# Optimization experiments

Measured on AMD Instinct MI355X. Metric: run time of the kernel, lower is better.

The kernel has to match this reference:

```python
import jax, jax.numpy as jnp
import numpy as np

N, M, P = 16, 4, 8
BSZ, T = 256, 256
STD_DYN, STD_OBS = 0.1, 0.1


def setup_inputs() -> dict:
    key = jax.random.key(0)
    ks = jax.random.split(key, 5)
    Y = jax.random.normal(ks[0], (BSZ, T, P), dtype=jnp.float32)
    U = jax.random.normal(ks[1], (BSZ, T, M), dtype=jnp.float32)
    # stable time-varying dynamics (spectral radius < 1)
    A_seq = 0.85 * jnp.eye(N, dtype=jnp.float32) + 0.02 * jax.random.normal(ks[2], (T, N, N), dtype=jnp.float32)
    B_seq = 0.1 * jax.random.normal(ks[3], (T, N, M), dtype=jnp.float32)
    C_seq = jax.random.normal(ks[4], (T, P, N), dtype=jnp.float32) / np.float32(np.sqrt(N))
    mu0 = jnp.zeros((N,), dtype=jnp.float32)
    Sigma0 = jnp.eye(N, dtype=jnp.float32)
    return dict(Y=Y, U=U, A_seq=A_seq, B_seq=B_seq, C_seq=C_seq, mu0=mu0, Sigma0=Sigma0)


def _sym(x):
    return 0.5 * (x + jnp.swapaxes(x, -1, -2))


def reference(Y, U, A_seq, B_seq, C_seq, mu0, Sigma0):
    B, T_, p = Y.shape
    n = mu0.shape[0]
    Q = (STD_DYN ** 2) * jnp.eye(n, dtype=Y.dtype)
    R = (STD_OBS ** 2) * jnp.eye(p, dtype=Y.dtype)
    I = jnp.eye(n, dtype=Y.dtype)
    Yt = jnp.swapaxes(Y, 0, 1)  # [T,B,p] time-major for scan
    Ut = jnp.swapaxes(U, 0, 1)  # [T,B,m]

    def filt_step(carry, xs):
        mu, Sig = carry                      # [B,n], [B,n,n]
        y_t, u_t, A, Bm, C = xs
        mu_pred = mu @ A.T + u_t @ Bm.T      # [B,n]
        Sig_pred = jnp.einsum('ij,bjk,lk->bil', A, Sig, A) + Q
        r = y_t - mu_pred @ C.T              # innovation [B,p]
        S = _sym(jnp.einsum('ij,bjk,lk->bil', C, Sig_pred, C) + R)
        PCT = Sig_pred @ C.T                 # [B,n,p]
        K = jnp.swapaxes(jnp.linalg.solve(S, jnp.swapaxes(PCT, -1, -2)), -1, -2)  # [B,n,p]
        mu_f = mu_pred + jnp.einsum('bnp,bp->bn', K, r)
        I_KC = I - K @ C                     # [B,n,n]
        Sig_f = _sym(jnp.einsum('bij,bjk,blk->bil', I_KC, Sig_pred, I_KC)
                     + jnp.einsum('bip,pq,bjq->bij', K, R, K))
        return (mu_f, Sig_f), (mu_f, Sig_f, mu_pred, Sig_pred)

    mu_init = jnp.broadcast_to(mu0, (B, n))
    Sig_init = jnp.broadcast_to(Sigma0, (B, n, n))
    _, (mus_f, Sigs_f, mus_p, Sigs_p) = jax.lax.scan(
        filt_step, (mu_init, Sig_init), (Yt, Ut, A_seq, B_seq, C_seq))

    def smooth_step(carry, xs):
        mu_next, Sig_next = carry            # smoothed t+1
        mu_f, Sig_f, mu_p_next, Sig_p_next, A_next = xs
        SfAT = jnp.einsum('bij,kj->bik', Sig_f, A_next)  # Sigma_t|t A_{t+1}^T
        J = jnp.swapaxes(jnp.linalg.solve(jnp.swapaxes(Sig_p_next, -1, -2),
                                          jnp.swapaxes(SfAT, -1, -2)), -1, -2)
        mu_s = mu_f + jnp.einsum('bij,bj->bi', J, mu_next - mu_p_next)
        Sig_s = _sym(Sig_f + jnp.einsum('bij,bjk,blk->bil', J, Sig_next - Sig_p_next, J))
        return (mu_s, Sig_s), (mu_s, Sig_s)

    carry0 = (mus_f[-1], Sigs_f[-1])
    xs = (mus_f[:-1], Sigs_f[:-1], mus_p[1:], Sigs_p[1:], A_seq[1:])
    _, (mus_s, Sigs_s) = jax.lax.scan(smooth_step, carry0, xs, reverse=True)
    mus_smooth = jnp.concatenate([mus_s, mus_f[-1:]], axis=0)    # [T,B,n]
    Sigs_smooth = jnp.concatenate([Sigs_s, Sigs_f[-1:]], axis=0)  # [T,B,n,n]

    return (jnp.swapaxes(mus_smooth, 0, 1),   # [B,T,n]
            jnp.swapaxes(Sigs_smooth, 0, 1),  # [B,T,n,n]
            jnp.swapaxes(mus_f, 0, 1),        # [B,T,n]
            jnp.swapaxes(Sigs_f, 0, 1))       # [B,T,n,n]
```

## Files before the change

kernel.cpp:

```cpp
#include <hip/hip_runtime.h>

#define NS 16
#define MD 4
#define PD 8
#define BB 256
#define TL 256
#define QV 0.01f
#define RV 0.01f
#define NCHF 256
#define WF   14
#define NCHS 256
#define WSS  14
#define CHM  8
#define NCHM 32
#define WMU  26

#define WSYNC() do { asm volatile("s_waitcnt lgkmcnt(0)" ::: "memory"); \
                     __builtin_amdgcn_sched_barrier(0); } while (0)

#define Z4 make_float4(0.f, 0.f, 0.f, 0.f)

__device__ __forceinline__ float f4c(const float4 v, int i) {
    return i == 0 ? v.x : i == 1 ? v.y : i == 2 ? v.z : v.w;
}

__global__ __launch_bounds__(256, 1) void kPre(
    const float* __restrict__ A_seq, const float* __restrict__ C_seq,
    float* __restrict__ E_ws, float* __restrict__ SQ_ws)
{
    const int t = blockIdx.x, tid = threadIdx.x;
    __shared__ float sA[16][17], sC[8][17];
    sA[tid >> 4][tid & 15] = A_seq[t * 256 + tid];
    if (tid < 128) sC[tid >> 4][tid & 15] = C_seq[t * 128 + tid];
    __syncthreads();
    if (tid < 128) {
        const int p = tid >> 4, j = tid & 15;
        float a = 0.f;
        #pragma unroll
        for (int k = 0; k < 16; ++k) a += sC[p][k] * sA[k][j];
        E_ws[t * 128 + tid] = a;
    } else if (tid < 192) {
        const int q2 = tid - 128, p = q2 >> 3, q = q2 & 7;
        float a = 0.f;
        #pragma unroll
        for (int k = 0; k < 16; ++k) a += sC[p][k] * sC[q][k];
        SQ_ws[t * 64 + q2] = QV * a + ((p == q) ? RV : 0.f);
    }
}

__global__ __launch_bounds__(64, 1) void kF3_warm(
    const float* __restrict__ A_seq, const float* __restrict__ C_seq,
    const float* __restrict__ E_ws, const float* __restrict__ SQ_ws,
    const float* __restrict__ Sig0,
    float* __restrict__ K_ws, float* __restrict__ Sigf_ws,
    float* __restrict__ Sigp_ws)
{
    const int tlo = blockIdx.x;
    int t0 = tlo - WF; if (t0 < 0) t0 = 0;
    const int nst = tlo + 1 - t0;

    const int l  = threadIdx.x;
    const int r  = l >> 2;
    const int q  = l & 3;
    const int c0 = q * 4;
    const int rc  = l >> 3;
    const int cc0 = (l & 7) * 2;
    const int c8  = l & 7;

    __shared__ float lA[2][16][20];
    __shared__ float lCc[2][8][20];
    __shared__ float lEe[2][8][20];
    __shared__ float lSQs[2][64];
    __shared__ float lSg[2][16][20];
    __shared__ float lT[16][20];
    __shared__ float lW[8][20];
    __shared__ float lCS[8][20];
    __shared__ float lS[64];
    __shared__ float lV[16][20];

    float4 sig4;
    if (t0 == 0) {
        sig4 = *(const float4*)(Sig0 + l * 4);
    } else {
        sig4 = make_float4(r == c0 ? 1.f : 0.f, r == c0 + 1 ? 1.f : 0.f,
                           r == c0 + 2 ? 1.f : 0.f, r == c0 + 3 ? 1.f : 0.f);
    }
    float4 a_c  = *(const float4*)(A_seq + t0 * 256 + l * 4);
    float2 cc_c = *(const float2*)(C_seq + t0 * 128 + l * 2);
    float2 e_c  = *(const float2*)(E_ws  + t0 * 128 + l * 2);
    float  sq_c = SQ_ws[t0 * 64 + l];

    for (int s = 0; s < nst; ++s) {
        const int t = t0 + s;
        const int pb = s & 1;
        const bool commit = (t == tlo);

        *(float4*)&lA[pb][r][c0]   = a_c;
        *(float2*)&lCc[pb][rc][cc0] = cc_c;
        *(float2*)&lEe[pb][rc][cc0] = e_c;
        lSQs[pb][l] = sq_c;
        *(float4*)&lSg[pb][r][c0]  = sig4;
        WSYNC();
        if (s + 1 < nst) {
            a_c  = *(const float4*)(A_seq + (t + 1) * 256 + l * 4);
            cc_c = *(const float2*)(C_seq + (t + 1) * 128 + l * 2);
            e_c  = *(const float2*)(E_ws  + (t + 1) * 128 + l * 2);
            sq_c = SQ_ws[(t + 1) * 64 + l];
        }

        float t4[4] = {0.f, 0.f, 0.f, 0.f};
        #pragma unroll
        for (int kk = 0; kk < 4; ++kk) {
            const float4 a4 = *(const float4*)&lA[pb][r][4 * kk];
            #pragma unroll
            for (int i2 = 0; i2 < 4; ++i2) {
                const float av = f4c(a4, i2);
                const float4 sv = *(const float4*)&lSg[pb][4 * kk + i2][c0];
                t4[0] += av * sv.x; t4[1] += av * sv.y;
                t4[2] += av * sv.z; t4[3] += av * sv.w;
            }
        }
        float w2x = 0.f, w2y = 0.f;
        {
            float4 er[4];
            #pragma unroll
            for (int kk = 0; kk < 4; ++kk) er[kk] = *(const float4*)&lEe[pb][rc][4 * kk];
            #pragma unroll
            for (int kk = 0; kk < 4; ++kk)
                #pragma unroll
                for (int i2 = 0; i2 < 4; ++i2) {
                    const float ev = f4c(er[kk], i2);
                    const float2 s2 = *(const float2*)&lSg[pb][4 * kk + i2][cc0];
                    w2x += ev * s2.x; w2y += ev * s2.y;
                }
        }
        *(float4*)&lT[r][c0]   = make_float4(t4[0], t4[1], t4[2], t4[3]);
        *(float2*)&lW[rc][cc0] = make_float2(w2x, w2y);
        WSYNC();

        float4 trr[4], wrow[4];
// ... 63 lines not shown
                    Lm[r2][c2] = s2 * Dinv[c2];
                }
            }
            float yv[8];
            #pragma unroll
            for (int c2 = 0; c2 < 8; ++c2) {
                float sAcc = lCS[c2][r];
                #pragma unroll
                for (int k2 = 0; k2 < 8; ++k2) if (k2 < c2) sAcc -= Lm[c2][k2] * yv[k2];
                yv[c2] = sAcc * Dinv[c2];
            }
            #pragma unroll
            for (int c2 = 7; c2 >= 0; --c2) {
                float sAcc = yv[c2];
                #pragma unroll
                for (int k2 = 0; k2 < 8; ++k2) if (k2 > c2) sAcc -= Lm[k2][c2] * x[k2];
                x[c2] = sAcc * Dinv[c2];
            }
        }
        float u[4] = { sp[0], sp[1], sp[2], sp[3] };
        #pragma unroll
        for (int p = 0; p < 8; ++p) {
            const float kv = x[p];
            const float4 cs4 = *(const float4*)&lCS[p][c0];
            u[0] -= kv * cs4.x; u[1] -= kv * cs4.y;
            u[2] -= kv * cs4.z; u[3] -= kv * cs4.w;
        }

        if (!commit) {
            sig4 = make_float4(u[0], u[1], u[2], u[3]);
        } else {
            if (q == 0)      *(float4*)(K_ws + t * 128 + r * 8)     = make_float4(x[0], x[1], x[2], x[3]);
            else if (q == 1) *(float4*)(K_ws + t * 128 + r * 8 + 4) = make_float4(x[4], x[5], x[6], x[7]);
            *(float4*)&lV[r][c0] = make_float4(u[0], u[1], u[2], u[3]);
            WSYNC();
            float o[4];
            #pragma unroll
            for (int i = 0; i < 4; ++i) o[i] = 0.5f * (u[i] + lV[c0 + i][r]);
            sig4 = make_float4(o[0], o[1], o[2], o[3]);
            *(float4*)(Sigf_ws + t * 256 + l * 4) = sig4;
        }
    }
}

__global__ __launch_bounds__(256, 1) void kBG(
    const float* __restrict__ A_seq, const float* __restrict__ B_seq,
    const float* __restrict__ C_seq, const float* __restrict__ K_ws,
    const float* __restrict__ Sigf_ws, const float* __restrict__ Sigp_ws,
    float* __restrict__ J_ws, float* __restrict__ G_ws,
    float* __restrict__ Bt2_ws)
{
    const int t = blockIdx.x, tid = threadIdx.x;
    const int i = tid >> 4, j = tid & 15;
    const bool doJ = (t < TL - 1);

    __shared__ float sA0[16][17], sCm[8][17], sKm[16][9], sBm[16][5];
    __shared__ float sCA[8][17], sCB[8][5];
    __shared__ float sSf[16][17], sA1[16][17], sFA[16][17];
    __shared__ float P[2][16][33];

    sA0[i][j] = A_seq[t * 256 + tid];
    if (tid < 128) {
        sCm[tid >> 4][tid & 15] = C_seq[t * 128 + tid];
        sKm[tid >> 3][tid & 7]  = K_ws[t * 128 + tid];
    }
    if (tid < 64) sBm[tid >> 2][tid & 3] = B_seq[t * 64 + tid];
    if (doJ) {
        sSf[i][j] = Sigf_ws[t * 256 + tid];
        sA1[i][j] = A_seq[(t + 1) * 256 + tid];
        P[0][i][j]      = Sigp_ws[(t + 1) * 256 + tid];
        P[0][i][j + 16] = (i == j) ? 1.f : 0.f;
    }
    __syncthreads();

    if (tid < 128) {
        const int p = tid >> 4, jj = tid & 15;
        float a = 0.f;
        #pragma unroll
        for (int k = 0; k < 16; ++k) a += sCm[p][k] * sA0[k][jj];
        sCA[p][jj] = a;
    } else if (tid < 160) {
        const int qq = tid - 128, p = qq >> 2, m = qq & 3;
        float a = 0.f;
        #pragma unroll
        for (int k = 0; k < 16; ++k) a += sCm[p][k] * sBm[k][m];
        sCB[p][m] = a;
    }
    if (doJ) {
        float fa = 0.f;
        #pragma unroll
        for (int k = 0; k < 16; ++k) fa += sSf[i][k] * sA1[j][k];
        sFA[i][j] = fa;
    }
    __syncthreads();

    float gv = sA0[i][j];
    #pragma unroll
    for (int p = 0; p < 8; ++p) gv -= sKm[i][p] * sCA[p][j];
    G_ws[t * 256 + tid] = gv;
    if (tid < 64) {
        const int ii = tid >> 2, m = tid & 3;
        float bv = sBm[ii][m];
        #pragma unroll
        for (int p = 0; p < 8; ++p) bv -= sKm[ii][p] * sCB[p][m];
        Bt2_ws[t * 64 + tid] = bv;
    }

    if (doJ) {
        #pragma unroll 1
        for (int k = 0; k < 16; ++k) {
            const int cur = k & 1, nxt = cur ^ 1;
            const float akk = P[cur][k][k];
            const float piv = 1.f / akk;
            const float rkj  = P[cur][k][j];
            const float rkj2 = P[cur][k][j + 16];
            if (i == k) {
                P[nxt][i][j]      = rkj * piv;
                P[nxt][i][j + 16] = rkj2 * piv;
            } else {
                const float f = P[cur][i][k] * piv;
                P[nxt][i][j]      = P[cur][i][j]      - f * rkj;
                P[nxt][i][j + 16] = P[cur][i][j + 16] - f * rkj2;
            }
            __syncthreads();
        }
        float acc = 0.f;
        #pragma unroll
        for (int k = 0; k < 16; ++k) acc += sFA[i][k] * P[0][k][16 + j];
        J_ws[t * 256 + tid] = acc;
    }
}

__global__ __launch_bounds__(256, 1) void kES3(
    const float* __restrict__ A_seq, const float* __restrict__ B_seq,
    const float* __restrict__ U, const float* __restrict__ Y,
    const float* __restrict__ mu0,
    const float* __restrict__ G_ws, const float* __restrict__ Bt2_ws,
    const float* __restrict__ K_ws, const float* __restrict__ Sigf_ws,
    const float* __restrict__ Sigp_ws, const float* __restrict__ J_ws,
    float* __restrict__ Sigs_ws, float* __restrict__ mus_f_out,
    float* __restrict__ mup_ws, float* __restrict__ Sigs_f_out)
{
    const int bid = blockIdx.x, tid = threadIdx.x;

    if (bid < NCHS) {
        if (tid < 64) {
            const int l   = tid;
            const int r   = l >> 2;
            const int c0  = (l & 3) * 4;
            const int tlo = bid;
            int tstart = tlo + WSS; if (tstart > 254) tstart = 254;

            __shared__ float sJ[2][16][20];
            __shared__ float sD[2][16][20];
            __shared__ float sT1[16][20];
            __shared__ float sV[16][20];

            float4 sS = *(const float4*)(Sigf_ws + (tstart + 1) * 256 + l * 4);
            if (tlo == 255) {
                *(float4*)(Sigs_ws + 255 * 256 + l * 4) = sS;
            }

            float4 j_c  = *(const float4*)(J_ws    + tstart * 256 + l * 4);
            float4 sp_c = *(const float4*)(Sigp_ws + (tstart + 1) * 256 + l * 4);
            float4 sf_c = *(const float4*)(Sigf_ws + tstart * 256 + l * 4);

            for (int t = tstart; t >= tlo; --t) {
                const int pb = t & 1;
                float4 d4 = make_float4(sS.x - sp_c.x, sS.y - sp_c.y,
                                        sS.z - sp_c.z, sS.w - sp_c.w);
                *(float4*)&sJ[pb][r][c0] = j_c;
                *(float4*)&sD[pb][r][c0] = d4;
                WSYNC();
                const float4 sf_use = sf_c;
// ... 17 lines not shown
                }
                *(float4*)&sT1[r][c0] = make_float4(a4[0], a4[1], a4[2], a4[3]);
                WSYNC();

                float4 t1r[4];
                #pragma unroll
                for (int kk = 0; kk < 4; ++kk) t1r[kk] = *(const float4*)&sT1[r][4 * kk];
                float v[4];
                #pragma unroll
                for (int i = 0; i < 4; ++i) {
                    float a = f4c(sf_use, i);
                    #pragma unroll
                    for (int kk = 0; kk < 4; ++kk) {
                        const float4 j4 = *(const float4*)&sJ[pb][c0 + i][4 * kk];
                        a += t1r[kk].x * j4.x + t1r[kk].y * j4.y
                           + t1r[kk].z * j4.z + t1r[kk].w * j4.w;
                    }
                    v[i] = a;
                }

                if (t > tlo) {
                    sS = make_float4(v[0], v[1], v[2], v[3]);
                } else {
                    *(float4*)&sV[r][c0] = make_float4(v[0], v[1], v[2], v[3]);
                    WSYNC();
                    float o[4];
                    #pragma unroll
                    for (int i = 0; i < 4; ++i) o[i] = 0.5f * (v[i] + sV[c0 + i][r]);
                    *(float4*)(Sigs_ws + t * 256 + l * 4) =
                        make_float4(o[0], o[1], o[2], o[3]);
                }
            }
        }
    } else if (bid < NCHS + NCHM * 16) {
        const int eb = bid - NCHS;
        const int ch = eb >> 4;
        const int gq = eb & 15;
        const int w  = tid >> 6;
        const int l  = tid & 63;
        const int g  = l >> 4;
        const int i  = l & 15;
        const int b  = (gq * 4 + w) * 4 + g;
        const int base = l & 48;
        const int tlo  = ch * CHM;
        int t0 = tlo - WMU; if (t0 < 0) t0 = 0;
        const int tend = tlo + CHM;

        float mu = (t0 == 0) ? mu0[i] : 0.f;

        float4 g_c[4], a_c[4] = {Z4, Z4, Z4, Z4}, k_c[2];
        float4 b_c = Z4, bt_c, u_c, y0_c, y1_c;
        {
            const float* Gb = G_ws + t0 * 256 + i * 16;
            #pragma unroll
            for (int kk = 0; kk < 4; ++kk) g_c[kk] = *(const float4*)(Gb + 4 * kk);
            if (t0 >= tlo) {
                const float* Ab = A_seq + t0 * 256 + i * 16;
                #pragma unroll
                for (int kk = 0; kk < 4; ++kk) a_c[kk] = *(const float4*)(Ab + 4 * kk);
                b_c = *(const float4*)(B_seq + t0 * 64 + i * 4);
            }
            k_c[0] = *(const float4*)(K_ws + t0 * 128 + i * 8);
            k_c[1] = *(const float4*)(K_ws + t0 * 128 + i * 8 + 4);
            bt_c = *(const float4*)(Bt2_ws + t0 * 64 + i * 4);
            u_c  = *(const float4*)(U + ((size_t)b * TL + t0) * MD);
            y0_c = *(const float4*)(Y + ((size_t)b * TL + t0) * PD);
            y1_c = *(const float4*)(Y + ((size_t)b * TL + t0) * PD + 4);
        }

        for (int t = t0; t < tend; ++t) {
            float4 g_n[4] = {Z4, Z4, Z4, Z4}, a_n[4] = {Z4, Z4, Z4, Z4};
            float4 k_n[2] = {Z4, Z4};
            float4 b_n = Z4, bt_n = Z4, u_n = Z4, y0_n = Z4, y1_n = Z4;
            if (t + 1 < tend) {
                const float* Gb = G_ws + (t + 1) * 256 + i * 16;
                #pragma unroll
                for (int kk = 0; kk < 4; ++kk) g_n[kk] = *(const float4*)(Gb + 4 * kk);
                if (t + 1 >= tlo) {
                    const float* Ab = A_seq + (t + 1) * 256 + i * 16;
                    #pragma unroll
                    for (int kk = 0; kk < 4; ++kk) a_n[kk] = *(const float4*)(Ab + 4 * kk);
                    b_n = *(const float4*)(B_seq + (t + 1) * 64 + i * 4);
                }
                k_n[0] = *(const float4*)(K_ws + (t + 1) * 128 + i * 8);
                k_n[1] = *(const float4*)(K_ws + (t + 1) * 128 + i * 8 + 4);
                bt_n = *(const float4*)(Bt2_ws + (t + 1) * 64 + i * 4);
                u_n  = *(const float4*)(U + ((size_t)b * TL + t + 1) * MD);
                y0_n = *(const float4*)(Y + ((size_t)b * TL + t + 1) * PD);
                y1_n = *(const float4*)(Y + ((size_t)b * TL + t + 1) * PD + 4);
            }

            const bool com = (t >= tlo);
            float sg0 = 0.f, sg1 = 0.f, sg2 = 0.f, sg3 = 0.f;
            float sa0 = 0.f, sa1 = 0.f, sa2 = 0.f, sa3 = 0.f;
            #pragma unroll
            for (int k4 = 0; k4 < 4; ++k4) {
                const float m0 = __shfl(mu, base + 4 * k4 + 0);
                const float m1 = __shfl(mu, base + 4 * k4 + 1);
                const float m2 = __shfl(mu, base + 4 * k4 + 2);
                const float m3 = __shfl(mu, base + 4 * k4 + 3);
                sg0 += f4c(g_c[k4], 0) * m0;
                sg1 += f4c(g_c[k4], 1) * m1;
                sg2 += f4c(g_c[k4], 2) * m2;
                sg3 += f4c(g_c[k4], 3) * m3;
                if (com) {
                    sa0 += f4c(a_c[k4], 0) * m0;
                    sa1 += f4c(a_c[k4], 1) * m1;
                    sa2 += f4c(a_c[k4], 2) * m2;
                    sa3 += f4c(a_c[k4], 3) * m3;
                }
            }
            float mf = (sg0 + sg1) + (sg2 + sg3);
            #pragma unroll
            for (int m = 0; m < 4; ++m) {
                mf += f4c(bt_c, m) * f4c(u_c, m);
                mf += f4c(k_c[0], m) * f4c(y0_c, m);
                mf += f4c(k_c[1], m) * f4c(y1_c, m);
            }
            if (com) {
                float mp = (sa0 + sa1) + (sa2 + sa3);
                #pragma unroll
                for (int m = 0; m < 4; ++m) mp += f4c(b_c, m) * f4c(u_c, m);
                mup_ws[((size_t)b * TL + t) * NS + i]    = mp;
                mus_f_out[((size_t)b * TL + t) * NS + i] = mf;
            }
            mu = mf;

            #pragma unroll
            for (int kk = 0; kk < 4; ++kk) { g_c[kk] = g_n[kk]; a_c[kk] = a_n[kk]; }
            k_c[0] = k_n[0]; k_c[1] = k_n[1];
            b_c = b_n; bt_c = bt_n; u_c = u_n; y0_c = y0_n; y1_c = y1_n;
        }
    } else {
        const size_t total = (size_t)BB * TL * 64;
        const int lb = bid - (NCHS + NCHM * 16);
        size_t idx = (size_t)lb * 256 + tid;
        const size_t stride = (size_t)1024 * 256;
        for (size_t x = idx; x < total; x += stride) {
            const size_t e4 = x & 63;
            const size_t t = (x >> 6) & 255;
            ((float4*)Sigs_f_out)[x] = ((const float4*)Sigf_ws)[t * 64 + e4];
        }
    }
}

__global__ __launch_bounds__(256, 1) void kFD(
    const float* __restrict__ mus_f, const float* __restrict__ mup_ws,
    const float* __restrict__ J_ws, float* __restrict__ mus_s,
    const float* __restrict__ Sigs_ws, float* __restrict__ Sigs_s_out)
{
    const int bid = blockIdx.x, tid = threadIdx.x;

    if (bid < NCHM * 16) {
        const int ch = bid >> 4;
        const int gq = bid & 15;
        const int w  = tid >> 6;
        const int l  = tid & 63;
        const int g  = l >> 4;
        const int i  = l & 15;
        const int b  = (gq * 4 + w) * 4 + g;
        const int base = l & 48;
        const int tlo = ch * CHM;
        const int thi = tlo + CHM - 1;
        int tstart = thi + WMU; if (tstart > 254) tstart = 254;

        float muS = mus_f[((size_t)b * TL + tstart + 1) * NS + i];
        if (thi == 255) mus_s[((size_t)b * TL + 255) * NS + i] = muS;

        float4 j_c[4];
        float f_c, p_c;
        #pragma unroll
        for (int kk = 0; kk < 4; ++kk)
            j_c[kk] = *(const float4*)(J_ws + tstart * 256 + i * 16 + 4 * kk);
        f_c = mus_f[((size_t)b * TL + tstart) * NS + i];
        p_c = mup_ws[((size_t)b * TL + tstart + 1) * NS + i];

        for (int t = tstart; t >= tlo; --t) {
            float4 j_n[4] = {Z4, Z4, Z4, Z4};
            float f_n = 0.f, p_n = 0.f;
            if (t > tlo) {
                #pragma unroll
                for (int kk = 0; kk < 4; ++kk)
                    j_n[kk] = *(const float4*)(J_ws + (t - 1) * 256 + i * 16 + 4 * kk);
                f_n = mus_f[((size_t)b * TL + t - 1) * NS + i];
                p_n = mup_ws[((size_t)b * TL + t) * NS + i];
            }

            const float d = muS - p_c;
            float q0 = 0.f, q1 = 0.f, q2 = 0.f, q3 = 0.f;
            #pragma unroll
            for (int k4 = 0; k4 < 4; ++k4) {
                q0 += f4c(j_c[k4], 0) * __shfl(d, base + 4 * k4 + 0);
                q1 += f4c(j_c[k4], 1) * __shfl(d, base + 4 * k4 + 1);
                q2 += f4c(j_c[k4], 2) * __shfl(d, base + 4 * k4 + 2);
                q3 += f4c(j_c[k4], 3) * __shfl(d, base + 4 * k4 + 3);
            }
            muS = f_c + ((q0 + q1) + (q2 + q3));
            if (t <= thi) mus_s[((size_t)b * TL + t) * NS + i] = muS;

            #pragma unroll
            for (int kk = 0; kk < 4; ++kk) j_c[kk] = j_n[kk];
            f_c = f_n; p_c = p_n;
        }
    } else {
        const size_t total = (size_t)BB * TL * 64;
        const int lb = bid - NCHM * 16;
        size_t idx = (size_t)lb * 256 + tid;
        const size_t stride = (size_t)1024 * 256;
        for (size_t x = idx; x < total; x += stride) {
            const size_t e4 = x & 63;
            const size_t t = (x >> 6) & 255;
            ((float4*)Sigs_s_out)[x] = ((const float4*)Sigs_ws)[t * 64 + e4];
        }
    }
}

extern "C" void kernel_launch(void* const* d_in, const int* in_sizes, int n_in,
                              void* d_out, int out_size, void* d_ws, size_t ws_size,
                              hipStream_t stream) {
    const float* Y     = (const float*)d_in[0];
    const float* U     = (const float*)d_in[1];
    const float* A_seq = (const float*)d_in[2];
    const float* B_seq = (const float*)d_in[3];
    const float* C_seq = (const float*)d_in[4];
    const float* mu0   = (const float*)d_in[5];
    const float* Sig0  = (const float*)d_in[6];

    float* out = (float*)d_out;
    const size_t nBT = (size_t)BB * TL;
    float* mus_s_out  = out;
    float* Sigs_s_out = mus_s_out + nBT * NS;
    float* mus_f_out  = Sigs_s_out + nBT * NS * NS;
    float* Sigs_f_out = mus_f_out + nBT * NS;

    float* w = (float*)d_ws;
    float* K_ws    = w;  w += TL * NS * PD;
    float* Sigf_ws = w;  w += TL * 256;
    float* Sigp_ws = w;  w += TL * 256;
    float* J_ws    = w;  w += TL * 256;
    float* Sigs_ws = w;  w += TL * 256;
    float* G_ws    = w;  w += TL * 256;
    float* Bt2_ws  = w;  w += TL * 64;
    float* E_ws    = w;  w += TL * 128;
    float* SQ_ws   = w;  w += TL * 64;
    float* mup_ws  = w;  w += nBT * NS;

    kPre    <<<TL, 256, 0, stream>>>(A_seq, C_seq, E_ws, SQ_ws);
    kF3_warm<<<NCHF, 64, 0, stream>>>(A_seq, C_seq, E_ws, SQ_ws, Sig0,
                                      K_ws, Sigf_ws, Sigp_ws);
    kBG     <<<TL, 256, 0, stream>>>(A_seq, B_seq, C_seq, K_ws, Sigf_ws, Sigp_ws,
                                     J_ws, G_ws, Bt2_ws);
    kES3    <<<NCHS + NCHM * 16 + 1024, 256, 0, stream>>>(A_seq, B_seq, U, Y, mu0,
        G_ws, Bt2_ws, K_ws, Sigf_ws, Sigp_ws, J_ws,
        Sigs_ws, mus_f_out, mup_ws, Sigs_f_out);
    kFD     <<<NCHM * 16 + 1024, 256, 0, stream>>>(mus_f_out, mup_ws, J_ws, mus_s_out,
                                                   Sigs_ws, Sigs_s_out);
}
```

Measured before the change: 120.5 us.

## Precompose 4-step transition products to shorten filter and smoother mean warm-up chains

Result: slower. 148.2 us (+22.9%).

```diff
diff --git a/kernel.cpp b/kernel.cpp
--- a/kernel.cpp
+++ b/kernel.cpp
@@ -11,9 +11,6 @@
 #define WF   14
 #define NCHS 256
 #define WSS  14
-#define CHM  8
-#define NCHM 32
-#define WMU  26
 
 #define WSYNC() do { asm volatile("s_waitcnt lgkmcnt(0)" ::: "memory"); \
                      __builtin_amdgcn_sched_barrier(0); } while (0)
@@ -95,11 +92,11 @@
         const int pb = s & 1;
         const bool commit = (t == tlo);
 
-        *(float4*)&lA[pb][r][c0]   = a_c;
+        *(float4*)&lA[pb][r][c0]    = a_c;
         *(float2*)&lCc[pb][rc][cc0] = cc_c;
         *(float2*)&lEe[pb][rc][cc0] = e_c;
         lSQs[pb][l] = sq_c;
-        *(float4*)&lSg[pb][r][c0]  = sig4;
+        *(float4*)&lSg[pb][r][c0]   = sig4;
         WSYNC();
         if (s + 1 < nst) {
             a_c  = *(const float4*)(A_seq + (t + 1) * 256 + l * 4);
@@ -313,8 +310,7 @@
         #pragma unroll 1
         for (int k = 0; k < 16; ++k) {
             const int cur = k & 1, nxt = cur ^ 1;
-            const float akk = P[cur][k][k];
-            const float piv = 1.f / akk;
+            const float piv = 1.f / P[cur][k][k];
             const float rkj  = P[cur][k][j];
             const float rkj2 = P[cur][k][j + 16];
             if (i == k) {
@@ -334,6 +330,128 @@
     }
 }
 
+__global__ __launch_bounds__(256, 1) void kComp(
+    const float* __restrict__ G_ws, const float* __restrict__ K_ws,
+    const float* __restrict__ Bt2_ws, const float* __restrict__ J_ws,
+    const float* __restrict__ Sigf_ws,
+    float* __restrict__ FG4_ws, float* __restrict__ FK_ws,
+    float* __restrict__ FB_ws, float* __restrict__ Mf_ws,
+    float* __restrict__ Sigs_f_out)
+{
+    const int bid = blockIdx.x, tid = threadIdx.x;
+
+    if (bid < 64) {
+        const int g = bid;
+        const int i = tid >> 4, j = tid & 15;
+        __shared__ float sG[4][16][17];
+        __shared__ float sK[4][16][9];
+        __shared__ float sB[4][16][5];
+        __shared__ float sP[2][16][17];
+
+        #pragma unroll
+        for (int s = 0; s < 4; ++s) sG[s][i][j] = G_ws[(4 * g + s) * 256 + tid];
+        if (tid < 128) {
+            #pragma unroll
+            for (int s = 0; s < 4; ++s) sK[s][tid >> 3][tid & 7] = K_ws[(4 * g + s) * 128 + tid];
+        } else if (tid < 192) {
+            const int t2 = tid - 128;
+            #pragma unroll
+            for (int s = 0; s < 4; ++s) sB[s][t2 >> 2][t2 & 3] = Bt2_ws[(4 * g + s) * 64 + t2];
+        }
+        __syncthreads();
+
+        if (tid < 128) FK_ws[g * 512 + 3 * 128 + tid] = sK[3][tid >> 3][tid & 7];
+        else if (tid < 192) { const int t2 = tid - 128; FB_ws[g * 256 + 3 * 64 + t2] = sB[3][t2 >> 2][t2 & 3]; }
+        float a = 0.f;
+        #pragma unroll
+        for (int k = 0; k < 16; ++k) a += sG[3][i][k] * sG[2][k][j];
+        sP[0][i][j] = a;
+        __syncthreads();
+
+        if (tid < 128) {
+            const int ii = tid >> 3, p = tid & 7;
+            float x2 = 0.f, x1 = 0.f;
+            #pragma unroll
+            for (int k = 0; k < 16; ++k) {
+                x2 += sG[3][ii][k] * sK[2][k][p];
+                x1 += sP[0][ii][k] * sK[1][k][p];
+            }
+            FK_ws[g * 512 + 2 * 128 + tid] = x2;
+            FK_ws[g * 512 + 1 * 128 + tid] = x1;
+        } else if (tid < 192) {
+            const int t2 = tid - 128, ii = t2 >> 2, m = t2 & 3;
+            float x2 = 0.f, x1 = 0.f;
+            #pragma unroll
+            for (int k = 0; k < 16; ++k) {
+                x2 += sG[3][ii][k] * sB[2][k][m];
+                x1 += sP[0][ii][k] * sB[1][k][m];
+            }
+            FB_ws[g * 256 + 2 * 64 + t2] = x2;
+            FB_ws[g * 256 + 1 * 64 + t2] = x1;
+        }
+        float a2 = 0.f;
+        #pragma unroll
+        for (int k = 0; k < 16; ++k) a2 += sP[0][i][k] * sG[1][k][j];
+        sP[1][i][j] = a2;
+        __syncthreads();
+
+        float a3 = 0.f;
+        #pragma unroll
+        for (int k = 0; k < 16; ++k) a3 += sP[1][i][k] * sG[0][k][j];
+        FG4_ws[g * 256 + tid] = a3;
+        if (tid < 128) {
+            const int ii = tid >> 3, p = tid & 7;
+            float x0 = 0.f;
+            #pragma unroll
+            for (int k = 0; k < 16; ++k) x0 += sP[1][ii][k] * sK[0][k][p];
+            FK_ws[g * 512 + tid] = x0;
+        } else if (tid < 192) {
+            const int t2 = tid - 128, ii = t2 >> 2, m = t2 & 3;
+            float x0 = 0.f;
+            #pragma unroll
+            for (int k = 0; k < 16; ++k) x0 += sP[1][ii][k] * sB[0][k][m];
+            FB_ws[g * 256 + t2] = x0;
+        }
+    } else if (bid < 128) {
+        const int g = bid - 64;
+        const int i = tid >> 4, j = tid & 15;
+        const int smax = (g == 63) ? 3 : 4;
+        __shared__ float sJ[4][16][17];
+        __shared__ float sP[2][16][17];
+        #pragma unroll
+        for (int s = 0; s < 4; ++s)
+            sJ[s][i][j] = (s < smax) ? J_ws[(4 * g + s) * 256 + tid] : 0.f;
+        __syncthreads();
+        Mf_ws[g * 1024 + tid] = sJ[0][i][j];
+        float a = 0.f;
+        #pragma unroll
+        for (int k = 0; k < 16; ++k) a += sJ[0][i][k] * sJ[1][k][j];
+        sP[0][i][j] = a;
+        Mf_ws[g * 1024 + 256 + tid] = a;
+        __syncthreads();
+        float a2 = 0.f;
+        #pragma unroll
+        for (int k = 0; k < 16; ++k) a2 += sP[0][i][k] * sJ[2][k][j];
+        sP[1][i][j] = a2;
+        Mf_ws[g * 1024 + 512 + tid] = a2;
+        __syncthreads();
+        float a3 = 0.f;
+        #pragma unroll
+        for (int k = 0; k < 16; ++k) a3 += sP[1][i][k] * sJ[3][k][j];
+        Mf_ws[g * 1024 + 768 + tid] = (g == 63) ? 0.f : a3;
+    } else {
+        const size_t total = (size_t)BB * TL * 64;
+        const int lb = bid - 128;
+        size_t idx = (size_t)lb * 256 + tid;
+        const size_t stride = (size_t)1024 * 256;
+        for (size_t x = idx; x < total; x += stride) {
+            const size_t e4 = x & 63;
+            const size_t t = (x >> 6) & 255;
+            ((float4*)Sigs_f_out)[x] = ((const float4*)Sigf_ws)[t * 64 + e4];
+        }
+    }
+}
+
 __global__ __launch_bounds__(256, 1) void kES3(
     const float* __restrict__ A_seq, const float* __restrict__ B_seq,
     const float* __restrict__ U, const float* __restrict__ Y,
@@ -341,8 +459,10 @@
     const float* __restrict__ G_ws, const float* __restrict__ Bt2_ws,
     const float* __restrict__ K_ws, const float* __restrict__ Sigf_ws,
     const float* __restrict__ Sigp_ws, const float* __restrict__ J_ws,
+    const float* __restrict__ FG4_ws, const float* __restrict__ FK_ws,
+    const float* __restrict__ FB_ws,
     float* __restrict__ Sigs_ws, float* __restrict__ mus_f_out,
-    float* __restrict__ mup_ws, float* __restrict__ Sigs_f_out)
+    float* __restrict__ mup_ws)
 {
     const int bid = blockIdx.x, tid = threadIdx.x;
 
@@ -426,179 +546,177 @@
                 }
             }
         }
-    } else if (bid < NCHS + NCHM * 16) {
+    } else {
         const int eb = bid - NCHS;
         const int ch = eb >> 4;
         const int gq = eb & 15;
         const int w  = tid >> 6;
         const int l  = tid & 63;
-        const int g  = l >> 4;
+        const int grp = l >> 4;
         const int i  = l & 15;
-        const int b  = (gq * 4 + w) * 4 + g;
+        const int b  = (gq * 4 + w) * 4 + grp;
         const int base = l & 48;
-        const int tlo  = ch * CHM;
-        int t0 = tlo - WMU; if (t0 < 0) t0 = 0;
-        const int tend = tlo + CHM;
-
-        float mu = (t0 == 0) ? mu0[i] : 0.f;
-
-        float4 g_c[4], a_c[4] = {Z4, Z4, Z4, Z4}, k_c[2];
-        float4 b_c = Z4, bt_c, u_c, y0_c, y1_c;
-        {
-            const float* Gb = G_ws + t0 * 256 + i * 16;
-            #pragma unroll
-            for (int kk = 0; kk < 4; ++kk) g_c[kk] = *(const float4*)(Gb + 4 * kk);
-            if (t0 >= tlo) {
-                const float* Ab = A_seq + t0 * 256 + i * 16;
-                #pragma unroll
-                for (int kk = 0; kk < 4; ++kk) a_c[kk] = *(const float4*)(Ab + 4 * kk);
-                b_c = *(const float4*)(B_seq + t0 * 64 + i * 4);
-            }
-            k_c[0] = *(const float4*)(K_ws + t0 * 128 + i * 8);
-            k_c[1] = *(const float4*)(K_ws + t0 * 128 + i * 8 + 4);
-            bt_c = *(const float4*)(Bt2_ws + t0 * 64 + i * 4);
-            u_c  = *(const float4*)(U + ((size_t)b * TL + t0) * MD);
-            y0_c = *(const float4*)(Y + ((size_t)b * TL + t0) * PD);
-            y1_c = *(const float4*)(Y + ((size_t)b * TL + t0) * PD + 4);
-        }
-
-        for (int t = t0; t < tend; ++t) {
-            float4 g_n[4] = {Z4, Z4, Z4, Z4}, a_n[4] = {Z4, Z4, Z4, Z4};
-            float4 k_n[2] = {Z4, Z4};
-            float4 b_n = Z4, bt_n = Z4, u_n = Z4, y0_n = Z4, y1_n = Z4;
-            if (t + 1 < tend) {
-                const float* Gb = G_ws + (t + 1) * 256 + i * 16;
-                #pragma unroll
-                for (int kk = 0; kk < 4; ++kk) g_n[kk] = *(const float4*)(Gb + 4 * kk);
-                if (t + 1 >= tlo) {
-                    const float* Ab = A_seq + (t + 1) * 256 + i * 16;
-                    #pragma unroll
-                    for (int kk = 0; kk < 4; ++kk) a_n[kk] = *(const float4*)(Ab + 4 * kk);
-                    b_n = *(const float4*)(B_seq + (t + 1) * 64 + i * 4);
-                }
-                k_n[0] = *(const float4*)(K_ws + (t + 1) * 128 + i * 8);
-                k_n[1] = *(const float4*)(K_ws + (t + 1) * 128 + i * 8 + 4);
-                bt_n = *(const float4*)(Bt2_ws + (t + 1) * 64 + i * 4);
-                u_n  = *(const float4*)(U + ((size_t)b * TL + t + 1) * MD);
-                y0_n = *(const float4*)(Y + ((size_t)b * TL + t + 1) * PD);
-                y1_n = *(const float4*)(Y + ((size_t)b * TL + t + 1) * PD + 4);
-            }
-
-            const bool com = (t >= tlo);
-            float sg0 = 0.f, sg1 = 0.f, sg2 = 0.f, sg3 = 0.f;
-            float sa0 = 0.f, sa1 = 0.f, sa2 = 0.f, sa3 = 0.f;
+        const int tlo = ch * 4;
+        const int g0  = (tlo >= 28) ? ((tlo - 28) >> 2) : 0;
+
+        float mu = (g0 == 0 && tlo <= 28) ? mu0[i] : 0.f;
+
+        for (int g2 = g0; g2 < ch; ++g2) {
+            float4 fg[4];
+            #pragma unroll
+            for (int kk = 0; kk < 4; ++kk)
+                fg[kk] = *(const float4*)(FG4_ws + g2 * 256 + i * 16 + 4 * kk);
+            float bias = 0.f;
+            #pragma unroll
+            for (int s = 0; s < 4; ++s) {
+                const int t = 4 * g2 + s;
+                const float4 fk0 = *(const float4*)(FK_ws + g2 * 512 + s * 128 + i * 8);
+                const float4 fk1 = *(const float4*)(FK_ws + g2 * 512 + s * 128 + i * 8 + 4);
+                const float4 fb  = *(const float4*)(FB_ws + g2 * 256 + s * 64 + i * 4);
+                const float4 y0 = *(const float4*)(Y + ((size_t)b * TL + t) * PD);
+                const float4 y1 = *(const float4*)(Y + ((size_t)b * TL + t) * PD + 4);
+                const float4 uu = *(const float4*)(U + ((size_t)b * TL + t) * MD);
+                #pragma unroll
+                for (int m = 0; m < 4; ++m)
+                    bias += f4c(fk0, m) * f4c(y0, m) + f4c(fk1, m) * f4c(y1, m)
+                          + f4c(fb, m) * f4c(uu, m);
+            }
+            float acc = bias;
+            #pragma unroll
+            for (int k4 = 0; k4 < 4; ++k4) {
+                acc += f4c(fg[k4], 0) * __shfl(mu, base + 4 * k4 + 0)
+                     + f4c(fg[k4], 1) * __shfl(mu, base + 4 * k4 + 1)
+                     + f4c(fg[k4], 2) * __shfl(mu, base + 4 * k4 + 2)
+                     + f4c(fg[k4], 3) * __shfl(mu, base + 4 * k4 + 3);
+            }
+            mu = acc;
+        }
+
+        #pragma unroll 1
+        for (int t = tlo; t < tlo + 4; ++t) {
+            float4 g_c[4], a_c[4];
+            #pragma unroll
+            for (int kk = 0; kk < 4; ++kk) {
+                g_c[kk] = *(const float4*)(G_ws  + t * 256 + i * 16 + 4 * kk);
+                a_c[kk] = *(const float4*)(A_seq + t * 256 + i * 16 + 4 * kk);
+            }
+            const float4 k0 = *(const float4*)(K_ws + t * 128 + i * 8);
+            const float4 k1 = *(const float4*)(K_ws + t * 128 + i * 8 + 4);
+            const float4 bb = *(const float4*)(B_seq + t * 64 + i * 4);
+            const float4 bt = *(const float4*)(Bt2_ws + t * 64 + i * 4);
+            const float4 uu = *(const float4*)(U + ((size_t)b * TL + t) * MD);
+            const float4 y0 = *(const float4*)(Y + ((size_t)b * TL + t) * PD);
+            const float4 y1 = *(const float4*)(Y + ((size_t)b * TL + t) * PD + 4);
+            float sg = 0.f, sa = 0.f;
             #pragma unroll
             for (int k4 = 0; k4 < 4; ++k4) {
                 const float m0 = __shfl(mu, base + 4 * k4 + 0);
                 const float m1 = __shfl(mu, base + 4 * k4 + 1);
                 const float m2 = __shfl(mu, base + 4 * k4 + 2);
                 const float m3 = __shfl(mu, base + 4 * k4 + 3);
-                sg0 += f4c(g_c[k4], 0) * m0;
-                sg1 += f4c(g_c[k4], 1) * m1;
-                sg2 += f4c(g_c[k4], 2) * m2;
-                sg3 += f4c(g_c[k4], 3) * m3;
-                if (com) {
-                    sa0 += f4c(a_c[k4], 0) * m0;
-                    sa1 += f4c(a_c[k4], 1) * m1;
-                    sa2 += f4c(a_c[k4], 2) * m2;
-                    sa3 += f4c(a_c[k4], 3) * m3;
-                }
-            }
-            float mf = (sg0 + sg1) + (sg2 + sg3);
+                sg += f4c(g_c[k4], 0) * m0 + f4c(g_c[k4], 1) * m1
+                    + f4c(g_c[k4], 2) * m2 + f4c(g_c[k4], 3) * m3;
+                sa += f4c(a_c[k4], 0) * m0 + f4c(a_c[k4], 1) * m1
+                    + f4c(a_c[k4], 2) * m2 + f4c(a_c[k4], 3) * m3;
+            }
+            float mp = sa, mf = sg;
             #pragma unroll
             for (int m = 0; m < 4; ++m) {
-                mf += f4c(bt_c, m) * f4c(u_c, m);
-                mf += f4c(k_c[0], m) * f4c(y0_c, m);
-                mf += f4c(k_c[1], m) * f4c(y1_c, m);
-            }
-            if (com) {
-                float mp = (sa0 + sa1) + (sa2 + sa3);
-                #pragma unroll
-                for (int m = 0; m < 4; ++m) mp += f4c(b_c, m) * f4c(u_c, m);
-                mup_ws[((size_t)b * TL + t) * NS + i]    = mp;
-                mus_f_out[((size_t)b * TL + t) * NS + i] = mf;
-            }
+                mp += f4c(bb, m) * f4c(uu, m);
+                mf += f4c(bt, m) * f4c(uu, m)
+                    + f4c(k0, m) * f4c(y0, m) + f4c(k1, m) * f4c(y1, m);
+            }
+            mup_ws[((size_t)b * TL + t) * NS + i]    = mp;
+            mus_f_out[((size_t)b * TL + t) * NS + i] = mf;
             mu = mf;
-
-            #pragma unroll
-            for (int kk = 0; kk < 4; ++kk) { g_c[kk] = g_n[kk]; a_c[kk] = a_n[kk]; }
-            k_c[0] = k_n[0]; k_c[1] = k_n[1];
-            b_c = b_n; bt_c = bt_n; u_c = u_n; y0_c = y0_n; y1_c = y1_n;
-        }
-    } else {
-        const size_t total = (size_t)BB * TL * 64;
-        const int lb = bid - (NCHS + NCHM * 16);
-        size_t idx = (size_t)lb * 256 + tid;
-        const size_t stride = (size_t)1024 * 256;
-        for (size_t x = idx; x < total; x += stride) {
-            const size_t e4 = x & 63;
-            const size_t t = (x >> 6) & 255;
-            ((float4*)Sigs_f_out)[x] = ((const float4*)Sigf_ws)[t * 64 + e4];
         }
     }
 }
 
 __global__ __launch_bounds__(256, 1) void kFD(
     const float* __restrict__ mus_f, const float* __restrict__ mup_ws,
-    const float* __restrict__ J_ws, float* __restrict__ mus_s,
+    const float* __restrict__ J_ws, const float* __restrict__ Mf_ws,
+    float* __restrict__ mus_s,
     const float* __restrict__ Sigs_ws, float* __restrict__ Sigs_s_out)
 {
     const int bid = blockIdx.x, tid = threadIdx.x;
 
-    if (bid < NCHM * 16) {
+    if (bid < 1024) {
         const int ch = bid >> 4;
         const int gq = bid & 15;
         const int w  = tid >> 6;
         const int l  = tid & 63;
-        const int g  = l >> 4;
+        const int grp = l >> 4;
         const int i  = l & 15;
-        const int b  = (gq * 4 + w) * 4 + g;
+        const int b  = (gq * 4 + w) * 4 + grp;
         const int base = l & 48;
-        const int tlo = ch * CHM;
-        const int thi = tlo + CHM - 1;
-        int tstart = thi + WMU; if (tstart > 254) tstart = 254;
-
-        float muS = mus_f[((size_t)b * TL + tstart + 1) * NS + i];
-        if (thi == 255) mus_s[((size_t)b * TL + 255) * NS + i] = muS;
-
-        float4 j_c[4];
-        float f_c, p_c;
-        #pragma unroll
-        for (int kk = 0; kk < 4; ++kk)
-            j_c[kk] = *(const float4*)(J_ws + tstart * 256 + i * 16 + 4 * kk);
-        f_c = mus_f[((size_t)b * TL + tstart) * NS + i];
-        p_c = mup_ws[((size_t)b * TL + tstart + 1) * NS + i];
-
+        const int tlo = ch * 4;
+        const size_t bb4 = (size_t)b * TL;
+
+        float muS;
+        int tstart;
+        if (ch == 63) {
+            muS = mus_f[(bb4 + 255) * NS + i];
+            mus_s[(bb4 + 255) * NS + i] = muS;
+            tstart = 254;
+        } else {
+            const int g_hi = (ch + 7 > 63) ? 63 : ch + 7;
+            muS = (g_hi < 63) ? mus_f[(bb4 + 4 * g_hi + 4) * NS + i] : 0.f;
+            for (int g2 = g_hi; g2 > ch; --g2) {
+                float4 mf1[4], mf2[4], mf3[4], mf4[4];
+                #pragma unroll
+                for (int kk = 0; kk < 4; ++kk) {
+                    mf1[kk] = *(const float4*)(Mf_ws + g2 * 1024 +       i * 16 + 4 * kk);
+                    mf2[kk] = *(const float4*)(Mf_ws + g2 * 1024 + 256 + i * 16 + 4 * kk);
+                    mf3[kk] = *(const float4*)(Mf_ws + g2 * 1024 + 512 + i * 16 + 4 * kk);
+                    mf4[kk] = *(const float4*)(Mf_ws + g2 * 1024 + 768 + i * 16 + 4 * kk);
+                }
+                const float f0 = mus_f[(bb4 + 4 * g2) * NS + i];
+                const float d1 = mus_f[(bb4 + 4 * g2 + 1) * NS + i] - mup_ws[(bb4 + 4 * g2 + 1) * NS + i];
+                const float d2 = mus_f[(bb4 + 4 * g2 + 2) * NS + i] - mup_ws[(bb4 + 4 * g2 + 2) * NS + i];
+                const float d3 = mus_f[(bb4 + 4 * g2 + 3) * NS + i] - mup_ws[(bb4 + 4 * g2 + 3) * NS + i];
+                const float p4 = (g2 < 63) ? mup_ws[(bb4 + 4 * g2 + 4) * NS + i] : 0.f;
+                const float dm = muS - p4;
+                float acc = f0;
+                #pragma unroll
+                for (int k4 = 0; k4 < 4; ++k4) {
+                    #pragma unroll
+                    for (int e = 0; e < 4; ++e) {
+                        const int jj = base + 4 * k4 + e;
+                        acc += f4c(mf1[k4], e) * __shfl(d1, jj)
+                             + f4c(mf2[k4], e) * __shfl(d2, jj)
+                             + f4c(mf3[k4], e) * __shfl(d3, jj)
+                             + f4c(mf4[k4], e) * __shfl(dm, jj);
+                    }
+                }
+                muS = acc;
+            }
+            tstart = tlo + 3;
+        }
+
+        #pragma unroll 1
         for (int t = tstart; t >= tlo; --t) {
-            float4 j_n[4] = {Z4, Z4, Z4, Z4};
-            float f_n = 0.f, p_n = 0.f;
-            if (t > tlo) {
-                #pragma unroll
-                for (int kk = 0; kk < 4; ++kk)
-                    j_n[kk] = *(const float4*)(J_ws + (t - 1) * 256 + i * 16 + 4 * kk);
-                f_n = mus_f[((size_t)b * TL + t - 1) * NS + i];
-                p_n = mup_ws[((size_t)b * TL + t) * NS + i];
-            }
-
-            const float d = muS - p_c;
-            float q0 = 0.f, q1 = 0.f, q2 = 0.f, q3 = 0.f;
+            float4 j_c[4];
+            #pragma unroll
+            for (int kk = 0; kk < 4; ++kk)
+                j_c[kk] = *(const float4*)(J_ws + t * 256 + i * 16 + 4 * kk);
+            const float f = mus_f[(bb4 + t) * NS + i];
+            const float p = mup_ws[(bb4 + t + 1) * NS + i];
+            const float d = muS - p;
+            float acc = f;
             #pragma unroll
             for (int k4 = 0; k4 < 4; ++k4) {
-                q0 += f4c(j_c[k4], 0) * __shfl(d, base + 4 * k4 + 0);
-                q1 += f4c(j_c[k4], 1) * __shfl(d, base + 4 * k4 + 1);
-                q2 += f4c(j_c[k4], 2) * __shfl(d, base + 4 * k4 + 2);
-                q3 += f4c(j_c[k4], 3) * __shfl(d, base + 4 * k4 + 3);
-            }
-            muS = f_c + ((q0 + q1) + (q2 + q3));
-            if (t <= thi) mus_s[((size_t)b * TL + t) * NS + i] = muS;
-
-            #pragma unroll
-            for (int kk = 0; kk < 4; ++kk) j_c[kk] = j_n[kk];
-            f_c = f_n; p_c = p_n;
+                acc += f4c(j_c[k4], 0) * __shfl(d, base + 4 * k4 + 0)
+                     + f4c(j_c[k4], 1) * __shfl(d, base + 4 * k4 + 1)
+                     + f4c(j_c[k4], 2) * __shfl(d, base + 4 * k4 + 2)
+                     + f4c(j_c[k4], 3) * __shfl(d, base + 4 * k4 + 3);
+            }
+            muS = acc;
+            mus_s[(bb4 + t) * NS + i] = muS;
         }
     } else {
         const size_t total = (size_t)BB * TL * 64;
-        const int lb = bid - NCHM * 16;
+        const int lb = bid - 1024;
         size_t idx = (size_t)lb * 256 + tid;
         const size_t stride = (size_t)1024 * 256;
         for (size_t x = idx; x < total; x += stride) {
@@ -637,6 +755,10 @@
     float* Bt2_ws  = w;  w += TL * 64;
     float* E_ws    = w;  w += TL * 128;
     float* SQ_ws   = w;  w += TL * 64;
+    float* FG4_ws  = w;  w += 64 * 256;
+    float* FK_ws   = w;  w += 64 * 512;
+    float* FB_ws   = w;  w += 64 * 256;
+    float* Mf_ws   = w;  w += 64 * 1024;
     float* mup_ws  = w;  w += nBT * NS;
 
     kPre    <<<TL, 256, 0, stream>>>(A_seq, C_seq, E_ws, SQ_ws);
@@ -644,9 +766,11 @@
                                       K_ws, Sigf_ws, Sigp_ws);
     kBG     <<<TL, 256, 0, stream>>>(A_seq, B_seq, C_seq, K_ws, Sigf_ws, Sigp_ws,
                                      J_ws, G_ws, Bt2_ws);
-    kES3    <<<NCHS + NCHM * 16 + 1024, 256, 0, stream>>>(A_seq, B_seq, U, Y, mu0,
-        G_ws, Bt2_ws, K_ws, Sigf_ws, Sigp_ws, J_ws,
-        Sigs_ws, mus_f_out, mup_ws, Sigs_f_out);
-    kFD     <<<NCHM * 16 + 1024, 256, 0, stream>>>(mus_f_out, mup_ws, J_ws, mus_s_out,
-                                                   Sigs_ws, Sigs_s_out);
+    kComp   <<<1152, 256, 0, stream>>>(G_ws, K_ws, Bt2_ws, J_ws, Sigf_ws,
+                                       FG4_ws, FK_ws, FB_ws, Mf_ws, Sigs_f_out);
+    kES3    <<<NCHS + 1024, 256, 0, stream>>>(A_seq, B_seq, U, Y, mu0,
+        G_ws, Bt2_ws, K_ws, Sigf_ws, Sigp_ws, J_ws, FG4_ws, FK_ws, FB_ws,
+        Sigs_ws, mus_f_out, mup_ws);
+    kFD     <<<2048, 256, 0, stream>>>(mus_f_out, mup_ws, J_ws, Mf_ws, mus_s_out,
+                                       Sigs_ws, Sigs_s_out);
 }
```

## Fuse gain/smoother-gain kernel into warm-started covariance filter kernel

Applied to the files above, without the earlier changes.

Result: no change. 118.7 us (-1.5%).

```diff
diff --git a/kernel.cpp b/kernel.cpp
--- a/kernel.cpp
+++ b/kernel.cpp
@@ -48,12 +48,13 @@
     }
 }
 
-__global__ __launch_bounds__(64, 1) void kF3_warm(
+__global__ __launch_bounds__(64, 1) void kF3X(
     const float* __restrict__ A_seq, const float* __restrict__ C_seq,
     const float* __restrict__ E_ws, const float* __restrict__ SQ_ws,
-    const float* __restrict__ Sig0,
+    const float* __restrict__ Sig0, const float* __restrict__ B_seq,
     float* __restrict__ K_ws, float* __restrict__ Sigf_ws,
-    float* __restrict__ Sigp_ws)
+    float* __restrict__ Sigp_ws, float* __restrict__ J_ws,
+    float* __restrict__ G_ws, float* __restrict__ Bt2_ws)
 {
     const int tlo = blockIdx.x;
     int t0 = tlo - WF; if (t0 < 0) t0 = 0;
@@ -77,6 +78,8 @@
     __shared__ float lCS[8][20];
     __shared__ float lS[64];
     __shared__ float lV[16][20];
+    __shared__ float lBs[64];
+    __shared__ float lAug[2][16][36];
 
     float4 sig4;
     if (t0 == 0) {
@@ -89,23 +92,30 @@
     float2 cc_c = *(const float2*)(C_seq + t0 * 128 + l * 2);
     float2 e_c  = *(const float2*)(E_ws  + t0 * 128 + l * 2);
     float  sq_c = SQ_ws[t0 * 64 + l];
+    float  b_sc = 0.f;
+    float4 a1_c = Z4;
+    float  xk[8];
 
     for (int s = 0; s < nst; ++s) {
         const int t = t0 + s;
         const int pb = s & 1;
         const bool commit = (t == tlo);
 
-        *(float4*)&lA[pb][r][c0]   = a_c;
+        *(float4*)&lA[pb][r][c0]    = a_c;
         *(float2*)&lCc[pb][rc][cc0] = cc_c;
         *(float2*)&lEe[pb][rc][cc0] = e_c;
         lSQs[pb][l] = sq_c;
-        *(float4*)&lSg[pb][r][c0]  = sig4;
+        *(float4*)&lSg[pb][r][c0]   = sig4;
         WSYNC();
         if (s + 1 < nst) {
             a_c  = *(const float4*)(A_seq + (t + 1) * 256 + l * 4);
             cc_c = *(const float2*)(C_seq + (t + 1) * 128 + l * 2);
             e_c  = *(const float2*)(E_ws  + (t + 1) * 128 + l * 2);
             sq_c = SQ_ws[(t + 1) * 64 + l];
+        } else {
+            b_sc = B_seq[tlo * 64 + l];
+            if (tlo < TL - 1)
+                a1_c = *(const float4*)(A_seq + (tlo + 1) * 256 + l * 4);
         }
 
         float t4[4] = {0.f, 0.f, 0.f, 0.f};
@@ -235,102 +245,131 @@
         } else {
             if (q == 0)      *(float4*)(K_ws + t * 128 + r * 8)     = make_float4(x[0], x[1], x[2], x[3]);
             else if (q == 1) *(float4*)(K_ws + t * 128 + r * 8 + 4) = make_float4(x[4], x[5], x[6], x[7]);
+            #pragma unroll
+            for (int p = 0; p < 8; ++p) xk[p] = x[p];
+
+            const float4 arow = *(const float4*)&lA[pb][r][c0];
+            float g4[4] = { arow.x, arow.y, arow.z, arow.w };
+            #pragma unroll
+            for (int p = 0; p < 8; ++p) {
+                const float4 ee = *(const float4*)&lEe[pb][p][c0];
+                g4[0] -= x[p] * ee.x; g4[1] -= x[p] * ee.y;
+                g4[2] -= x[p] * ee.z; g4[3] -= x[p] * ee.w;
+            }
+            *(float4*)(G_ws + t * 256 + l * 4) = make_float4(g4[0], g4[1], g4[2], g4[3]);
+
             *(float4*)&lV[r][c0] = make_float4(u[0], u[1], u[2], u[3]);
+            lBs[l] = b_sc;
             WSYNC();
             float o[4];
             #pragma unroll
             for (int i = 0; i < 4; ++i) o[i] = 0.5f * (u[i] + lV[c0 + i][r]);
             sig4 = make_float4(o[0], o[1], o[2], o[3]);
             *(float4*)(Sigf_ws + t * 256 + l * 4) = sig4;
+
+            {
+                float bt = lBs[l];
+                #pragma unroll
+                for (int p = 0; p < 8; ++p) {
+                    float cb = 0.f;
+                    #pragma unroll
+                    for (int k = 0; k < 16; ++k) cb += lCc[pb][p][k] * lBs[k * 4 + q];
+                    bt -= x[p] * cb;
+                }
+                Bt2_ws[t * 64 + l] = bt;
+            }
         }
     }
-}
-
-__global__ __launch_bounds__(256, 1) void kBG(
-    const float* __restrict__ A_seq, const float* __restrict__ B_seq,
-    const float* __restrict__ C_seq, const float* __restrict__ K_ws,
-    const float* __restrict__ Sigf_ws, const float* __restrict__ Sigp_ws,
-    float* __restrict__ J_ws, float* __restrict__ G_ws,
-    float* __restrict__ Bt2_ws)
-{
-    const int t = blockIdx.x, tid = threadIdx.x;
-    const int i = tid >> 4, j = tid & 15;
-    const bool doJ = (t < TL - 1);
-
-    __shared__ float sA0[16][17], sCm[8][17], sKm[16][9], sBm[16][5];
-    __shared__ float sCA[8][17], sCB[8][5];
-    __shared__ float sSf[16][17], sA1[16][17], sFA[16][17];
-    __shared__ float P[2][16][33];
-
-    sA0[i][j] = A_seq[t * 256 + tid];
-    if (tid < 128) {
-        sCm[tid >> 4][tid & 15] = C_seq[t * 128 + tid];
-        sKm[tid >> 3][tid & 7]  = K_ws[t * 128 + tid];
-    }
-    if (tid < 64) sBm[tid >> 2][tid & 3] = B_seq[t * 64 + tid];
-    if (doJ) {
-        sSf[i][j] = Sigf_ws[t * 256 + tid];
-        sA1[i][j] = A_seq[(t + 1) * 256 + tid];
-        P[0][i][j]      = Sigp_ws[(t + 1) * 256 + tid];
-        P[0][i][j + 16] = (i == j) ? 1.f : 0.f;
-    }
-    __syncthreads();
-
-    if (tid < 128) {
-        const int p = tid >> 4, jj = tid & 15;
-        float a = 0.f;
-        #pragma unroll
-        for (int k = 0; k < 16; ++k) a += sCm[p][k] * sA0[k][jj];
-        sCA[p][jj] = a;
-    } else if (tid < 160) {
-        const int qq = tid - 128, p = qq >> 2, m = qq & 3;
-        float a = 0.f;
-        #pragma unroll
-        for (int k = 0; k < 16; ++k) a += sCm[p][k] * sBm[k][m];
-        sCB[p][m] = a;
-    }
-    if (doJ) {
-        float fa = 0.f;
-        #pragma unroll
-        for (int k = 0; k < 16; ++k) fa += sSf[i][k] * sA1[j][k];
-        sFA[i][j] = fa;
-    }
-    __syncthreads();
-
-    float gv = sA0[i][j];
-    #pragma unroll
-    for (int p = 0; p < 8; ++p) gv -= sKm[i][p] * sCA[p][j];
-    G_ws[t * 256 + tid] = gv;
-    if (tid < 64) {
-        const int ii = tid >> 2, m = tid & 3;
-        float bv = sBm[ii][m];
-        #pragma unroll
-        for (int p = 0; p < 8; ++p) bv -= sKm[ii][p] * sCB[p][m];
-        Bt2_ws[t * 64 + tid] = bv;
-    }
-
-    if (doJ) {
+
+    if (tlo < TL - 1) {
+        const int pb2 = nst & 1;
+        *(float4*)&lSg[pb2][r][c0] = sig4;
+        *(float4*)&lA[pb2][r][c0]  = a1_c;
+        WSYNC();
+
+        float t2[4] = {0.f, 0.f, 0.f, 0.f};
+        #pragma unroll
+        for (int kk = 0; kk < 4; ++kk) {
+            const float4 a4 = *(const float4*)&lA[pb2][r][4 * kk];
+            #pragma unroll
+            for (int i2 = 0; i2 < 4; ++i2) {
+                const float av = f4c(a4, i2);
+                const float4 sv2 = *(const float4*)&lSg[pb2][4 * kk + i2][c0];
+                t2[0] += av * sv2.x; t2[1] += av * sv2.y;
+                t2[2] += av * sv2.z; t2[3] += av * sv2.w;
+            }
+        }
+        float fa[4];
+        #pragma unroll
+        for (int i = 0; i < 4; ++i) {
+            float a = 0.f;
+            #pragma unroll
+            for (int kk = 0; kk < 4; ++kk) {
+                const float4 sf4 = *(const float4*)&lSg[pb2][r][4 * kk];
+                const float4 a4  = *(const float4*)&lA[pb2][c0 + i][4 * kk];
+                a += sf4.x * a4.x + sf4.y * a4.y + sf4.z * a4.z + sf4.w * a4.w;
+            }
+            fa[i] = a;
+        }
+        *(float4*)&lT[r][c0] = make_float4(t2[0], t2[1], t2[2], t2[3]);
+        *(float4*)&lV[r][c0] = make_float4(fa[0], fa[1], fa[2], fa[3]);
+        WSYNC();
+
+        float sp2[4];
+        #pragma unroll
+        for (int i = 0; i < 4; ++i) {
+            float a = (r == c0 + i) ? QV : 0.f;
+            #pragma unroll
+            for (int kk = 0; kk < 4; ++kk) {
+                const float4 tt = *(const float4*)&lT[r][4 * kk];
+                const float4 a4 = *(const float4*)&lA[pb2][c0 + i][4 * kk];
+                a += tt.x * a4.x + tt.y * a4.y + tt.z * a4.z + tt.w * a4.w;
+            }
+            sp2[i] = a;
+        }
+        *(float4*)&lAug[0][r][c0] = make_float4(sp2[0], sp2[1], sp2[2], sp2[3]);
+        *(float4*)&lAug[0][r][16 + c0] =
+            make_float4(r == c0 ? 1.f : 0.f, r == c0 + 1 ? 1.f : 0.f,
+                        r == c0 + 2 ? 1.f : 0.f, r == c0 + 3 ? 1.f : 0.f);
+        WSYNC();
+
         #pragma unroll 1
         for (int k = 0; k < 16; ++k) {
             const int cur = k & 1, nxt = cur ^ 1;
-            const float akk = P[cur][k][k];
-            const float piv = 1.f / akk;
-            const float rkj  = P[cur][k][j];
-            const float rkj2 = P[cur][k][j + 16];
-            if (i == k) {
-                P[nxt][i][j]      = rkj * piv;
-                P[nxt][i][j + 16] = rkj2 * piv;
+            const float piv = 1.f / lAug[cur][k][k];
+            const float4 rk  = *(const float4*)&lAug[cur][k][c0];
+            const float4 rk2 = *(const float4*)&lAug[cur][k][16 + c0];
+            float4 o1, o2;
+            if (r == k) {
+                o1 = make_float4(rk.x * piv,  rk.y * piv,  rk.z * piv,  rk.w * piv);
+                o2 = make_float4(rk2.x * piv, rk2.y * piv, rk2.z * piv, rk2.w * piv);
             } else {
-                const float f = P[cur][i][k] * piv;
-                P[nxt][i][j]      = P[cur][i][j]      - f * rkj;
-                P[nxt][i][j + 16] = P[cur][i][j + 16] - f * rkj2;
-            }
-            __syncthreads();
-        }
-        float acc = 0.f;
-        #pragma unroll
-        for (int k = 0; k < 16; ++k) acc += sFA[i][k] * P[0][k][16 + j];
-        J_ws[t * 256 + tid] = acc;
+                const float f = lAug[cur][r][k] * piv;
+                const float4 w1 = *(const float4*)&lAug[cur][r][c0];
+                const float4 w2 = *(const float4*)&lAug[cur][r][16 + c0];
+                o1 = make_float4(w1.x - f * rk.x,  w1.y - f * rk.y,
+                                 w1.z - f * rk.z,  w1.w - f * rk.w);
+                o2 = make_float4(w2.x - f * rk2.x, w2.y - f * rk2.y,
+                                 w2.z - f * rk2.z, w2.w - f * rk2.w);
+            }
+            *(float4*)&lAug[nxt][r][c0]      = o1;
+            *(float4*)&lAug[nxt][r][16 + c0] = o2;
+            WSYNC();
+        }
+
+        float j4[4] = {0.f, 0.f, 0.f, 0.f};
+        #pragma unroll
+        for (int kk = 0; kk < 4; ++kk) {
+            const float4 fv = *(const float4*)&lV[r][4 * kk];
+            #pragma unroll
+            for (int i2 = 0; i2 < 4; ++i2) {
+                const float v = f4c(fv, i2);
+                const float4 p4 = *(const float4*)&lAug[0][4 * kk + i2][16 + c0];
+                j4[0] += v * p4.x; j4[1] += v * p4.y;
+                j4[2] += v * p4.z; j4[3] += v * p4.w;
+            }
+        }
+        *(float4*)(J_ws + tlo * 256 + l * 4) = make_float4(j4[0], j4[1], j4[2], j4[3]);
     }
 }
 
@@ -639,14 +678,12 @@
     float* SQ_ws   = w;  w += TL * 64;
     float* mup_ws  = w;  w += nBT * NS;
 
-    kPre    <<<TL, 256, 0, stream>>>(A_seq, C_seq, E_ws, SQ_ws);
-    kF3_warm<<<NCHF, 64, 0, stream>>>(A_seq, C_seq, E_ws, SQ_ws, Sig0,
-                                      K_ws, Sigf_ws, Sigp_ws);
-    kBG     <<<TL, 256, 0, stream>>>(A_seq, B_seq, C_seq, K_ws, Sigf_ws, Sigp_ws,
-                                     J_ws, G_ws, Bt2_ws);
-    kES3    <<<NCHS + NCHM * 16 + 1024, 256, 0, stream>>>(A_seq, B_seq, U, Y, mu0,
+    kPre <<<TL, 256, 0, stream>>>(A_seq, C_seq, E_ws, SQ_ws);
+    kF3X <<<NCHF, 64, 0, stream>>>(A_seq, C_seq, E_ws, SQ_ws, Sig0, B_seq,
+                                   K_ws, Sigf_ws, Sigp_ws, J_ws, G_ws, Bt2_ws);
+    kES3 <<<NCHS + NCHM * 16 + 1024, 256, 0, stream>>>(A_seq, B_seq, U, Y, mu0,
         G_ws, Bt2_ws, K_ws, Sigf_ws, Sigp_ws, J_ws,
         Sigs_ws, mus_f_out, mup_ws, Sigs_f_out);
-    kFD     <<<NCHM * 16 + 1024, 256, 0, stream>>>(mus_f_out, mup_ws, J_ws, mus_s_out,
-                                                   Sigs_ws, Sigs_s_out);
+    kFD  <<<NCHM * 16 + 1024, 256, 0, stream>>>(mus_f_out, mup_ws, J_ws, mus_s_out,
+                                                Sigs_ws, Sigs_s_out);
 }
```
